# Optimization experiments

Hardware: AMD Instinct MI355X
Metric: run time of the kernel (lower is better)

## Reference

```python
import jax, jax.numpy as jnp
import numpy as np

C = 768
TEMB = 512
HID = int(C * 2.0)  # prompt_mlp hidden
K = max(1, int(C * 0.5))  # top-k channels = 384


def silu(x):
    return x * jax.nn.sigmoid(x)


def conv1x1(h, W, b):
    # h: [b,c,H,W], W: [o,c], b: [o]
    return jnp.einsum('bchw,oc->bohw', h, W) + b[None, :, None, None]


def setup_inputs() -> dict:
    key = jax.random.key(0)
    ks = jax.random.split(key, 20)
    s = 0.02
    return {
        'x': jax.random.normal(ks[0], (16, C, 64, 64), jnp.float32),
        'temb': jax.random.normal(ks[1], (16, TEMB), jnp.float32),
        'W_ts': jax.random.normal(ks[2], (2 * C, TEMB), jnp.float32) * s,
        'b_ts': jnp.zeros((2 * C,), jnp.float32),
        'W_tp': jax.random.normal(ks[3], (C, TEMB), jnp.float32) * s,
        'b_tp': jnp.zeros((C,), jnp.float32),
        'W_m1': jax.random.normal(ks[4], (HID, 2 * C), jnp.float32) * s,
        'b_m1': jnp.zeros((HID,), jnp.float32),
        'W_m2': jax.random.normal(ks[5], (C, HID), jnp.float32) * s,
        'b_m2': jnp.zeros((C,), jnp.float32),
        'Wq': jax.random.normal(ks[6], (C, C), jnp.float32) * s,
        'bq': jnp.zeros((C,), jnp.float32),
        'Wk': jax.random.normal(ks[7], (C, C), jnp.float32) * s,
        'bk': jnp.zeros((C,), jnp.float32),
        'Wv': jax.random.normal(ks[8], (C, C), jnp.float32) * s,
        'bv': jnp.zeros((C,), jnp.float32),
        'Wo': jax.random.normal(ks[9], (C, C), jnp.float32) * s,
        'bo': jnp.zeros((C,), jnp.float32),
    }


def reference(x, temb, W_ts, b_ts, W_tp, b_tp, W_m1, b_m1, W_m2, b_m2,
              Wq, bq, Wk, bk, Wv, bv, Wo, bo):
    b, c, H, W = x.shape
    # TimeScaleShift
    ss = silu(temb) @ W_ts.T + b_ts                       # [b, 2c]
    scale, shift = jnp.split(ss, 2, axis=1)
    h = x * (1 + scale[:, :, None, None]) + shift[:, :, None, None]
    # prompt
    gap = h.mean(axis=(2, 3))                             # [b, c]
    tp = silu(temb) @ W_tp.T + b_tp                       # [b, c]
    p = jnp.concatenate([gap, tp], axis=1)                # [b, 2c]
    prompt = silu(p @ W_m1.T + b_m1) @ W_m2.T + b_m2      # [b, c]
    # top-k channel selection
    _, idx = jax.lax.top_k(prompt, K)                     # [b, K]
    bi = jnp.arange(b)[:, None]
    # 1x1 convs then gather selected channels
    q = conv1x1(h, Wq, bq)[bi, idx].reshape(b, K, H * W)
    kf = conv1x1(h, Wk, bk)[bi, idx].reshape(b, K, H * W)
    v = conv1x1(h, Wv, bv)[bi, idx].reshape(b, K, H * W)
    # channel attention
    attn = jax.nn.softmax(jnp.einsum('bkn,bln->bkl', q, kf) * (K ** -0.5), axis=-1)
    out = jnp.einsum('bkl,bln->bkn', attn, v).reshape(b, K, H, W)
    # scatter back into full channel space
    out_full = jnp.zeros_like(h).at[bi, idx].set(out)
    return conv1x1(out_full, Wo, bo)
```

## Files before the change

kernel.cpp:

```cpp
#include <hip/hip_runtime.h>

#define NB 16
#define NC 768
#define NT 512
#define NH 1536
#define KS 384
#define NPX 4096

typedef __bf16 bfx8 __attribute__((ext_vector_type(8)));
typedef float fx4 __attribute__((ext_vector_type(4)));
typedef unsigned short u16;
typedef unsigned short usv4 __attribute__((ext_vector_type(4)));

__device__ __forceinline__ u16 f2bf(float f) {
  unsigned u = __builtin_bit_cast(unsigned, f);
  u += 0x7FFFu + ((u >> 16) & 1u);
  return (u16)(u >> 16);
}

__global__ void k_trans_mean(const float* __restrict__ x, u16* __restrict__ xT,
                             float* __restrict__ parts) {
  __shared__ float ld[64][65];
  int p0 = blockIdx.x * 64, c0 = blockIdx.y * 64, b = blockIdx.z;
  int t = threadIdx.x;
#pragma unroll
  for (int s = 0; s < 16; ++s) {
    int id = t + 256 * s;
    int i = id >> 6, j = id & 63;
    ld[i][j] = x[(size_t)(b * NC + c0 + i) * NPX + p0 + j];
  }
  __syncthreads();
#pragma unroll
  for (int s = 0; s < 16; ++s) {
    int id = t + 256 * s;
    int j = id >> 6, i = id & 63;
    xT[(size_t)(b * NPX + p0 + j) * NC + c0 + i] = f2bf(ld[i][j]);
  }
  if (t < 64) {
    float s = 0.f;
    for (int j = 0; j < 64; ++j) s += ld[t][j];
    parts[(size_t)(b * NC + c0 + t) * 64 + blockIdx.x] = s;
  }
}

__global__ void k_mean_fin(const float* __restrict__ parts, float* __restrict__ xmean) {
  int id = blockIdx.x * 256 + threadIdx.x;
  if (id >= NB * NC) return;
  float s = 0.f;
  for (int j = 0; j < 64; ++j) s += parts[(size_t)id * 64 + j];
  xmean[id] = s * (1.f / 4096.f);
}

__global__ void k_silu(const float* __restrict__ temb, float* __restrict__ st) {
  int id = blockIdx.x * 256 + threadIdx.x;
  if (id < NB * NT) { float v = temb[id]; st[id] = v / (1.f + expf(-v)); }
}

__global__ void k_mlp8(const float* __restrict__ W, const float* __restrict__ bias,
                       const float* __restrict__ X, float* __restrict__ Y,
                       int len, int nj, int ostride, int obase, int dosilu) {
  __shared__ float Xs[8 * 1537];
  int t = threadIdx.x, lane = t & 63, w = t >> 6;
  int b0 = blockIdx.y * 8;
  int ldx = len + 1;
  for (int id = t; id < 8 * len; id += 256) {
    int bb = id / len, s = id - bb * len;
    Xs[bb * ldx + s] = X[(size_t)(b0 + bb) * len + s];
  }
  __syncthreads();
  for (int i = 0; i < 4; ++i) {
    int j = blockIdx.x * 16 + i * 4 + w;
    if (j < nj) {
      float acc[8] = {0, 0, 0, 0, 0, 0, 0, 0};
      for (int s = lane; s < len; s += 64) {
        float wv = W[(size_t)j * len + s];
#pragma unroll
        for (int bb = 0; bb < 8; ++bb) acc[bb] += wv * Xs[bb * ldx + s];
      }
#pragma unroll
      for (int bb = 0; bb < 8; ++bb) {
        float r = acc[bb];
#pragma unroll
        for (int m = 32; m; m >>= 1) r += __shfl_xor(r, m);
        if (lane == 0) {
          r += bias[j];
          if (dosilu) r = r / (1.f + expf(-r));
          Y[(size_t)(b0 + bb) * ostride + obase + j] = r;
        }
      }
    }
  }
}

__global__ void k_assemble_p(const float* __restrict__ Y1, const float* __restrict__ xmean,
                             float* __restrict__ p) {
  int id = blockIdx.x * 256 + threadIdx.x;
  if (id >= NB * NC) return;
  int b = id / NC, c = id - b * NC;
  const float* yb = Y1 + (size_t)b * 2304;
  p[(size_t)b * 1536 + c] = xmean[id] * (1.f + yb[c]) + yb[768 + c];
  p[(size_t)b * 1536 + 768 + c] = yb[1536 + c];
}

__global__ void k_topk(const float* __restrict__ prompt, int* __restrict__ idx) {
  __shared__ float pr[NC];
  int b = blockIdx.x, t = threadIdx.x;
  for (int c = t; c < NC; c += 256) pr[c] = prompt[(size_t)b * NC + c];
  __syncthreads();
  for (int c = t; c < NC; c += 256) {
    float v = pr[c];
    int r = 0;
    for (int c2 = 0; c2 < NC; ++c2) {
      float v2 = pr[c2];
      r += (v2 > v) || (v2 == v && c2 < c);
    }
    if (r < KS) idx[b * KS + r] = c;
  }
}

__global__ void k_fold(const int* __restrict__ idx, const float* __restrict__ Y1,
                       const float* __restrict__ Wq, const float* __restrict__ bq,
                       const float* __restrict__ Wk, const float* __restrict__ bk,
                       const float* __restrict__ Wv, const float* __restrict__ bv,
                       u16* __restrict__ Aq, float* __restrict__ biasq) {
  __shared__ float red[3 * 256];
  int k = blockIdx.x, b = blockIdx.y, t = threadIdx.x;
  int row = idx[b * KS + k];
  const float* yb = Y1 + (size_t)b * 2304;
  u16* aq = Aq + (size_t)b * 1152 * NC;
  float dq = 0.f, dk = 0.f, dv = 0.f;
  for (int c = t; c < NC; c += 256) {
    float sc = 1.f + yb[c], sh = yb[768 + c];
    float wq = Wq[(size_t)row * NC + c];
    float wk = Wk[(size_t)row * NC + c];
    float wv = Wv[(size_t)row * NC + c];
    aq[(size_t)k * NC + c] = f2bf(wq * sc);
    aq[(size_t)(KS + k) * NC + c] = f2bf(wk * sc);
    aq[(size_t)(2 * KS + k) * NC + c] = f2bf(wv * sc);
    dq += wq * sh; dk += wk * sh; dv += wv * sh;
  }
  red[t] = dq; red[256 + t] = dk; red[512 + t] = dv;
  __syncthreads();
  for (int s = 128; s; s >>= 1) {
    if (t < s) {
      red[t] += red[t + s];
      red[256 + t] += red[256 + t + s];
      red[512 + t] += red[512 + t + s];
    }
    __syncthreads();
  }
  if (t == 0) {
    biasq[b * 1152 + k] = bq[row] + red[0];
    biasq[b * 1152 + KS + k] = bk[row] + red[256];
    biasq[b * 1152 + 2 * KS + k] = bv[row] + red[512];
  }
}

__global__ void k_gather_wo(const int* __restrict__ idx, const float* __restrict__ Wo,
                            u16* __restrict__ WoSel) {
  __shared__ int il[KS];
  int b = blockIdx.y, t = threadIdx.x;
  for (int k = t; k < KS; k += 256) il[k] = idx[b * KS + k];
  __syncthreads();
  int o0 = blockIdx.x * 8;
  for (int oo = 0; oo < 8; ++oo) {
    int o = o0 + oo;
    const float* wr = Wo + (size_t)o * NC;
    u16* dst = WoSel + ((size_t)b * NC + o) * KS;
    for (int k = t; k < KS; k += 256) dst[k] = f2bf(wr[il[k]]);
  }
}

__global__ void k_softmax(const float* __restrict__ S, u16* __restrict__ At) {
  __shared__ float sh[2];
  int kk = blockIdx.x, b = blockIdx.y, t = threadIdx.x;
  const float* srow = S + ((size_t)b * KS + kk) * KS;
  float v[3];
#pragma unroll
  for (int i = 0; i < 3; ++i) v[i] = srow[t + 128 * i];
  float m = fmaxf(fmaxf(v[0], v[1]), v[2]);
#pragma unroll
  for (int s = 32; s; s >>= 1) m = fmaxf(m, __shfl_xor(m, s));
  if ((t & 63) == 0) sh[t >> 6] = m;
  __syncthreads();
  m = fmaxf(sh[0], sh[1]);
  float e[3];
  float sum = 0.f;
#pragma unroll
  for (int i = 0; i < 3; ++i) { e[i] = expf(v[i] - m); sum += e[i]; }
#pragma unroll
  for (int s = 32; s; s >>= 1) sum += __shfl_xor(sum, s);
  __syncthreads();
  if ((t & 63) == 0) sh[t >> 6] = sum;
  __syncthreads();
  sum = sh[0] + sh[1];
  float inv = 1.f / sum;
#pragma unroll
  for (int i = 0; i < 3; ++i) {
    int l = t + 128 * i;
    At[((size_t)b * KS + l) * KS + kk] = f2bf(e[i] * inv);
  }
}

#define LDK 72

template <int EPI>
__global__ __launch_bounds__(256, 2) void gemm_bt(
    const u16* __restrict__ A, const u16* __restrict__ Bt, size_t sA, size_t sB,
    int ldA, int ldB, int K, const float* __restrict__ bias,
    float* __restrict__ outF, u16* __restrict__ outU, u16* __restrict__ outU2, float scale) {
  __shared__ u16 As[128 * LDK];
  __shared__ u16 Bs[128 * LDK];
  int b = blockIdx.z;
  int m0 = blockIdx.y * 128, n0 = blockIdx.x * 128;
  const u16* Ab = A + (size_t)b * sA;
  const u16* Bb = Bt + (size_t)b * sB;
  int t = threadIdx.x, lane = t & 63, w = t >> 6;
  int wm = (w >> 1) * 64, wn = (w & 1) * 64;
  int r16 = lane & 15, g = lane >> 4;

  fx4 acc[4][4] = {};

  for (int k0 = 0; k0 < K; k0 += 64) {
#pragma unroll
    for (int s = 0; s < 4; ++s) {
      int id = t + 256 * s;
      int row = id >> 3, c8 = (id & 7) * 8;
      *(int4*)&As[row * LDK + c8] = *(const int4*)(Ab + (size_t)(m0 + row) * ldA + k0 + c8);
      *(int4*)&Bs[row * LDK + c8] = *(const int4*)(Bb + (size_t)(n0 + row) * ldB + k0 + c8);
    }
    __syncthreads();
#pragma unroll
    for (int kk = 0; kk < 2; ++kk) {
      bfx8 af[4], bfr[4];
#pragma unroll
      for (int i = 0; i < 4; ++i) {
        af[i] = *(const bfx8*)&As[(wm + i * 16 + r16) * LDK + kk * 32 + g * 8];
        bfr[i] = *(const bfx8*)&Bs[(wn + i * 16 + r16) * LDK + kk * 32 + g * 8];
      }
#pragma unroll
      for (int i = 0; i < 4; ++i)
#pragma unroll
        for (int j = 0; j < 4; ++j)
          acc[i][j] = __builtin_amdgcn_mfma_f32_16x16x32_bf16(af[i], bfr[j], acc[i][j], 0, 0, 0);
    }
    __syncthreads();
  }

#pragma unroll
  for (int i = 0; i < 4; ++i) {
#pragma unroll
    for (int j = 0; j < 4; ++j) {
      int row = m0 + wm + i * 16 + g * 4;
      int col = n0 + wn + j * 16 + r16;
      fx4 v = acc[i][j];
      if constexpr (EPI == 0) {
        const float* bi = bias + b * 1152;
        if (row < 768) {
#pragma unroll
          for (int r = 0; r < 4; ++r)
            outU[((size_t)b * 768 + row + r) * 4096 + col] = f2bf(v[r] + bi[row + r]);
        } else {
          usv4 pk;
#pragma unroll
          for (int r = 0; r < 4; ++r) pk[r] = f2bf(v[r] + bi[row + r]);
          *(usv4*)&outU2[((size_t)b * 4096 + col) * 384 + (row - 768)] = pk;
        }
      } else if constexpr (EPI == 1) {
#pragma unroll
        for (int r = 0; r < 4; ++r)
          outF[((size_t)b * 384 + row + r) * 384 + col] = v[r] * scale;
      } else if constexpr (EPI == 2) {
#pragma unroll
        for (int r = 0; r < 4; ++r)
          outU[((size_t)b * 768 + row + r) * 384 + col] = f2bf(v[r]);
      } else {
#pragma unroll
        for (int r = 0; r < 4; ++r)
          outF[((size_t)b * 768 + row + r) * 4096 + col] = v[r] + bias[row + r];
      }
    }
  }
}

__global__ void k_sentinel(float* out, int n) {
  int id = blockIdx.x * 256 + threadIdx.x;
  if (id < n) out[id] = 12345.0f;
}

extern "C" void kernel_launch(void* const* d_in, const int* in_sizes, int n_in,
                              void* d_out, int out_size, void* d_ws, size_t ws_size,
                              hipStream_t stream) {
  const float* x    = (const float*)d_in[0];
  const float* temb = (const float*)d_in[1];
  const float* W_ts = (const float*)d_in[2];
  const float* b_ts = (const float*)d_in[3];
  const float* W_tp = (const float*)d_in[4];
  const float* b_tp = (const float*)d_in[5];
  const float* W_m1 = (const float*)d_in[6];
  const float* b_m1 = (const float*)d_in[7];
  const float* W_m2 = (const float*)d_in[8];
  const float* b_m2 = (const float*)d_in[9];
  const float* Wq = (const float*)d_in[10];
  const float* bq = (const float*)d_in[11];
  const float* Wk = (const float*)d_in[12];
  const float* bk = (const float*)d_in[13];
  const float* Wv = (const float*)d_in[14];
  const float* bv = (const float*)d_in[15];
  const float* Wo = (const float*)d_in[16];
  const float* bo = (const float*)d_in[17];
  float* out = (float*)d_out;

  char* base = (char*)d_ws;
  size_t off = 0;
  auto alloc = [&](size_t bytes) -> char* {
    char* pp = base + off;
    off += (bytes + 255) & ~(size_t)255;
    return pp;
  };
  u16* xT     = (u16*)alloc((size_t)NB * NPX * NC * 2);
  u16* qk     = (u16*)alloc((size_t)NB * 768 * NPX * 2);
  u16* vT     = (u16*)alloc((size_t)NB * NPX * KS * 2);
  u16* Aq     = (u16*)alloc((size_t)NB * 1152 * NC * 2);
  u16* WoS    = (u16*)alloc((size_t)NB * NC * KS * 2);
  float* parts  = (float*)alloc((size_t)NB * NC * 64 * 4);
  float* xmean  = (float*)alloc((size_t)NB * NC * 4);
  float* Y1     = (float*)alloc((size_t)NB * 2304 * 4);
  float* st     = (float*)alloc((size_t)NB * NT * 4);
  float* p      = (float*)alloc((size_t)NB * 1536 * 4);
  float* hid    = (float*)alloc((size_t)NB * 1536 * 4);
  float* pr     = (float*)alloc((size_t)NB * NC * 4);
  int*   idx    = (int*)alloc((size_t)NB * KS * 4);
  float* biasq  = (float*)alloc((size_t)NB * 1152 * 4);

  if (off > ws_size) {
    k_sentinel<<<(out_size + 255) / 256, 256, 0, stream>>>(out, out_size);
    return;
  }

  float* S = (float*)xT;
  u16* At  = (u16*)((char*)xT + 16u * 1024 * 1024);
  u16* Mm  = (u16*)((char*)xT + 24u * 1024 * 1024);

  k_trans_mean<<<dim3(64, 12, NB), 256, 0, stream>>>(x, xT, parts);
  k_mean_fin<<<(NB * NC + 255) / 256, 256, 0, stream>>>(parts, xmean);
  k_silu<<<(NB * NT + 255) / 256, 256, 0, stream>>>(temb, st);
  k_mlp8<<<dim3(96, 2), 256, 0, stream>>>(W_ts, b_ts, st, Y1, 512, 1536, 2304, 0, 0);
  k_mlp8<<<dim3(48, 2), 256, 0, stream>>>(W_tp, b_tp, st, Y1, 512, 768, 2304, 1536, 0);
  k_assemble_p<<<(NB * NC + 255) / 256, 256, 0, stream>>>(Y1, xmean, p);
  k_mlp8<<<dim3(96, 2), 256, 0, stream>>>(W_m1, b_m1, p, hid, 1536, 1536, 1536, 0, 1);
  k_mlp8<<<dim3(48, 2), 256, 0, stream>>>(W_m2, b_m2, hid, pr, 1536, 768, 768, 0, 0);
  k_topk<<<NB, 256, 0, stream>>>(pr, idx);
  k_fold<<<dim3(KS, NB), 256, 0, stream>>>(idx, Y1, Wq, bq, Wk, bk, Wv, bv, Aq, biasq);
  k_gather_wo<<<dim3(96, NB), 256, 0, stream>>>(idx, Wo, WoS);

  gemm_bt<0><<<dim3(32, 9, NB), 256, 0, stream>>>(
      Aq, xT, (size_t)1152 * NC, (size_t)NPX * NC, NC, NC, NC, biasq, nullptr, qk, vT, 0.f);
  gemm_bt<1><<<dim3(3, 3, NB), 256, 0, stream>>>(
      qk, qk + (size_t)KS * NPX, (size_t)768 * NPX, (size_t)768 * NPX, NPX, NPX, NPX,
      nullptr, S, nullptr, nullptr, 0.05103103630798287f);
  k_softmax<<<dim3(KS, NB), 128, 0, stream>>>(S, At);
  gemm_bt<2><<<dim3(3, 6, NB), 256, 0, stream>>>(
      WoS, At, (size_t)NC * KS, (size_t)KS * KS, KS, KS, KS, nullptr, nullptr, Mm, nullptr, 0.f);
  gemm_bt<3><<<dim3(32, 6, NB), 256, 0, stream>>>(
      Mm, vT, (size_t)NC * KS, (size_t)NPX * KS, KS, KS, KS, bo, out, nullptr, nullptr, 0.f);
}
```

Measured before the change: 717.4 us.

## Split-K the QK^T GEMM and load GEMM tiles via direct global-to-LDS

The QK^T score GEMM had only 144 blocks with a long K=4096 reduction, so it is now split four ways along K. Each part writes partial scores to its own buffer, and the softmax kernel sums the four partials before normalising. All GEMMs also switch from register-staged int4 tile loads to global_load_lds direct-to-LDS copies, dropping the padded LDS stride. The unpadded layout may add LDS bank conflicts on fragment reads, and the split adds partial-sum traffic to softmax.

```diff
diff --git a/kernel.cpp b/kernel.cpp
--- a/kernel.cpp
+++ b/kernel.cpp
@@ -6,6 +6,7 @@
 #define NH 1536
 #define KS 384
 #define NPX 4096
+#define BK 64
 
 typedef __bf16 bfx8 __attribute__((ext_vector_type(8)));
 typedef float fx4 __attribute__((ext_vector_type(4)));
@@ -16,6 +17,12 @@
   unsigned u = __builtin_bit_cast(unsigned, f);
   u += 0x7FFFu + ((u >> 16) & 1u);
   return (u16)(u >> 16);
+}
+
+__device__ __forceinline__ void gload16(const u16* g, u16* l) {
+  __builtin_amdgcn_global_load_lds(
+      (const __attribute__((address_space(1))) unsigned int*)g,
+      (__attribute__((address_space(3))) unsigned int*)l, 16, 0, 0);
 }
 
 __global__ void k_trans_mean(const float* __restrict__ x, u16* __restrict__ xT,
@@ -171,13 +178,17 @@
   }
 }
 
-__global__ void k_softmax(const float* __restrict__ S, u16* __restrict__ At) {
+__global__ void k_softmax(const float* __restrict__ Sp, u16* __restrict__ At) {
   __shared__ float sh[2];
   int kk = blockIdx.x, b = blockIdx.y, t = threadIdx.x;
-  const float* srow = S + ((size_t)b * KS + kk) * KS;
+  const size_t stride = (size_t)NB * KS * KS;
+  const float* srow = Sp + ((size_t)b * KS + kk) * KS;
   float v[3];
 #pragma unroll
-  for (int i = 0; i < 3; ++i) v[i] = srow[t + 128 * i];
+  for (int i = 0; i < 3; ++i) {
+    int l = t + 128 * i;
+    v[i] = srow[l] + srow[stride + l] + srow[2 * stride + l] + srow[3 * stride + l];
+  }
   float m = fmaxf(fmaxf(v[0], v[1]), v[2]);
 #pragma unroll
   for (int s = 32; s; s >>= 1) m = fmaxf(m, __shfl_xor(m, s));
@@ -202,16 +213,23 @@
   }
 }
 
-#define LDK 72
-
 template <int EPI>
 __global__ __launch_bounds__(256, 2) void gemm_bt(
     const u16* __restrict__ A, const u16* __restrict__ Bt, size_t sA, size_t sB,
-    int ldA, int ldB, int K, const float* __restrict__ bias,
+    int ldA, int ldB, int K, int ksplit, const float* __restrict__ bias,
     float* __restrict__ outF, u16* __restrict__ outU, u16* __restrict__ outU2, float scale) {
-  __shared__ u16 As[128 * LDK];
-  __shared__ u16 Bs[128 * LDK];
-  int b = blockIdx.z;
+  __shared__ u16 As[128 * BK];
+  __shared__ u16 Bs[128 * BK];
+  int bz = blockIdx.z;
+  int b = bz, kbeg = 0, kend = K;
+  if (ksplit > 1) {
+    b = bz / ksplit;
+    int part = bz - b * ksplit;
+    int kl = K / ksplit;
+    kbeg = part * kl;
+    kend = kbeg + kl;
+    outF += (size_t)part * NB * KS * KS;
+  }
   int m0 = blockIdx.y * 128, n0 = blockIdx.x * 128;
   const u16* Ab = A + (size_t)b * sA;
   const u16* Bb = Bt + (size_t)b * sB;
@@ -219,24 +237,29 @@
   int wm = (w >> 1) * 64, wn = (w & 1) * 64;
   int r16 = lane & 15, g = lane >> 4;
 
+  int srow = w * 32 + (lane >> 3);
+  int scol = (lane & 7) * 8;
+  const u16* Ag = Ab + (size_t)(m0 + srow) * ldA + kbeg + scol;
+  const u16* Bg = Bb + (size_t)(n0 + srow) * ldB + kbeg + scol;
+  u16* Asl = &As[(w * 32) * BK];
+  u16* Bsl = &Bs[(w * 32) * BK];
+
   fx4 acc[4][4] = {};
 
-  for (int k0 = 0; k0 < K; k0 += 64) {
-#pragma unroll
-    for (int s = 0; s < 4; ++s) {
-      int id = t + 256 * s;
-      int row = id >> 3, c8 = (id & 7) * 8;
-      *(int4*)&As[row * LDK + c8] = *(const int4*)(Ab + (size_t)(m0 + row) * ldA + k0 + c8);
-      *(int4*)&Bs[row * LDK + c8] = *(const int4*)(Bb + (size_t)(n0 + row) * ldB + k0 + c8);
-    }
+  for (int k0 = kbeg; k0 < kend; k0 += BK) {
+#pragma unroll
+    for (int s = 0; s < 4; ++s) gload16(Ag + (size_t)s * 8 * ldA, Asl + s * 8 * BK);
+#pragma unroll
+    for (int s = 0; s < 4; ++s) gload16(Bg + (size_t)s * 8 * ldB, Bsl + s * 8 * BK);
+    Ag += BK; Bg += BK;
     __syncthreads();
 #pragma unroll
     for (int kk = 0; kk < 2; ++kk) {
       bfx8 af[4], bfr[4];
 #pragma unroll
       for (int i = 0; i < 4; ++i) {
-        af[i] = *(const bfx8*)&As[(wm + i * 16 + r16) * LDK + kk * 32 + g * 8];
-        bfr[i] = *(const bfx8*)&Bs[(wn + i * 16 + r16) * LDK + kk * 32 + g * 8];
+        af[i] = *(const bfx8*)&As[(wm + i * 16 + r16) * BK + kk * 32 + g * 8];
+        bfr[i] = *(const bfx8*)&Bs[(wn + i * 16 + r16) * BK + kk * 32 + g * 8];
       }
 #pragma unroll
       for (int i = 0; i < 4; ++i)
@@ -338,9 +361,9 @@
     return;
   }
 
-  float* S = (float*)xT;
-  u16* At  = (u16*)((char*)xT + 16u * 1024 * 1024);
-  u16* Mm  = (u16*)((char*)xT + 24u * 1024 * 1024);
+  float* Sp = (float*)xT;
+  u16* At  = (u16*)((char*)xT + 40u * 1024 * 1024);
+  u16* Mm  = (u16*)((char*)xT + 48u * 1024 * 1024);
 
   k_trans_mean<<<dim3(64, 12, NB), 256, 0, stream>>>(x, xT, parts);
   k_mean_fin<<<(NB * NC + 255) / 256, 256, 0, stream>>>(parts, xmean);
@@ -355,13 +378,13 @@
   k_gather_wo<<<dim3(96, NB), 256, 0, stream>>>(idx, Wo, WoS);
 
   gemm_bt<0><<<dim3(32, 9, NB), 256, 0, stream>>>(
-      Aq, xT, (size_t)1152 * NC, (size_t)NPX * NC, NC, NC, NC, biasq, nullptr, qk, vT, 0.f);
-  gemm_bt<1><<<dim3(3, 3, NB), 256, 0, stream>>>(
-      qk, qk + (size_t)KS * NPX, (size_t)768 * NPX, (size_t)768 * NPX, NPX, NPX, NPX,
-      nullptr, S, nullptr, nullptr, 0.05103103630798287f);
-  k_softmax<<<dim3(KS, NB), 128, 0, stream>>>(S, At);
+      Aq, xT, (size_t)1152 * NC, (size_t)NPX * NC, NC, NC, NC, 1, biasq, nullptr, qk, vT, 0.f);
+  gemm_bt<1><<<dim3(3, 3, NB * 4), 256, 0, stream>>>(
+      qk, qk + (size_t)KS * NPX, (size_t)768 * NPX, (size_t)768 * NPX, NPX, NPX, NPX, 4,
+      nullptr, Sp, nullptr, nullptr, 0.05103103630798287f);
+  k_softmax<<<dim3(KS, NB), 128, 0, stream>>>(Sp, At);
   gemm_bt<2><<<dim3(3, 6, NB), 256, 0, stream>>>(
-      WoS, At, (size_t)NC * KS, (size_t)KS * KS, KS, KS, KS, nullptr, nullptr, Mm, nullptr, 0.f);
+      WoS, At, (size_t)NC * KS, (size_t)KS * KS, KS, KS, KS, 1, nullptr, nullptr, Mm, nullptr, 0.f);
   gemm_bt<3><<<dim3(32, 6, NB), 256, 0, stream>>>(
-      Mm, vT, (size_t)NC * KS, (size_t)NPX * KS, KS, KS, KS, bo, out, nullptr, nullptr, 0.f);
-}
+      Mm, vT, (size_t)NC * KS, (size_t)NPX * KS, KS, KS, KS, 1, bo, out, nullptr, nullptr, 0.f);
+}
```

New measurement: 642.4 us. 1.12x faster.
